# Kernel tuning notes

Hardware: AMD Instinct MI355X
Metric: run time of the kernel (lower is better)

The kernel has to match this reference:

```python
import jax, jax.numpy as jnp
import numpy as np

N_HEADS = 16
EMBED_DIM = 1024

def setup_inputs() -> dict:
    key = jax.random.key(0)
    ks = jax.random.split(key, 5)
    C = EMBED_DIM
    s = 0.02
    return {
        "x": jax.random.normal(ks[0], (4, 2048, C), dtype=jnp.float32),
        "W_attn": jax.random.normal(ks[1], (C, 3 * C), dtype=jnp.float32) * s,
        "b_attn": jnp.zeros((3 * C,), dtype=jnp.float32),
        "W_proj": jax.random.normal(ks[2], (C, C), dtype=jnp.float32) * s,
        "b_proj": jnp.zeros((C,), dtype=jnp.float32),
    }

def reference(x, W_attn, b_attn, W_proj, b_proj):
    B, T, C = x.shape
    H = N_HEADS
    hd = C // H
    qkv = x @ W_attn + b_attn                      # [B,T,3C]
    q, k, v = jnp.split(qkv, 3, axis=-1)
    # [B,T,C] -> [B,H,T,hd]
    q = q.reshape(B, T, H, hd).transpose(0, 2, 1, 3)
    k = k.reshape(B, T, H, hd).transpose(0, 2, 1, 3)
    v = v.reshape(B, T, H, hd).transpose(0, 2, 1, 3)
    scale = 1.0 / np.sqrt(hd).astype(np.float32)
    att = jnp.einsum("bhqd,bhkd->bhqk", q, k) * scale   # [B,H,T,T]
    causal = jnp.tril(jnp.ones((T, T), dtype=bool))
    att = jnp.where(causal[None, None], att, -jnp.inf)
    att = jax.nn.softmax(att, axis=-1)
    y = jnp.einsum("bhqk,bhkd->bhqd", att, v)            # [B,H,T,hd]
    y = y.transpose(0, 2, 1, 3).reshape(B, T, C)
    return y @ W_proj + b_proj
```

## Files before the change

### kernel.cpp

```cpp
#include <hip/hip_runtime.h>
#include <stdint.h>

#define T_ 2048
#define C_ 1024
#define H_ 16
#define HD_ 64

typedef __attribute__((ext_vector_type(8))) short bf16x8;
typedef __attribute__((ext_vector_type(4))) float f32x4;

#define EXP2F(x) __builtin_amdgcn_exp2f(x)

__device__ __forceinline__ unsigned short f2b(float f) {
  union { float f; unsigned u; } v; v.f = f;
  return (unsigned short)((v.u + 0x7fffu + ((v.u >> 16) & 1u)) >> 16);
}

__global__ void cvt_f32_bf16(const float* __restrict__ in, unsigned short* __restrict__ out, int n4) {
  int stride = gridDim.x * blockDim.x;
  for (int i = blockIdx.x * blockDim.x + threadIdx.x; i < n4; i += stride) {
    float4 v = ((const float4*)in)[i];
    ushort4 o;
    o.x = f2b(v.x); o.y = f2b(v.y); o.z = f2b(v.z); o.w = f2b(v.w);
    ((ushort4*)out)[i] = o;
  }
}

__global__ void transpose_cvt(const float* __restrict__ in, unsigned short* __restrict__ out, int K, int N) {
  __shared__ float tile[32][33];
  int k0 = blockIdx.x * 32, n0 = blockIdx.y * 32;
  int tx = threadIdx.x & 31, ty = threadIdx.x >> 5;
#pragma unroll
  for (int i = 0; i < 4; ++i)
    tile[ty + i*8][tx] = in[(size_t)(k0 + ty + i*8) * N + n0 + tx];
  __syncthreads();
#pragma unroll
  for (int i = 0; i < 4; ++i)
    out[(size_t)(n0 + ty + i*8) * K + k0 + tx] = f2b(tile[tx][ty + i*8]);
}

#define GL16(g, l) __builtin_amdgcn_global_load_lds((const __attribute__((address_space(1))) void*)(g), (__attribute__((address_space(3))) void*)(l), 16, 0, 0)

template<int EPI>
__global__ __launch_bounds__(256) void gemm128(
    const unsigned short* __restrict__ A,
    const unsigned short* __restrict__ Bt,
    const float* __restrict__ bias,
    float* __restrict__ outF,
    unsigned short* __restrict__ outQ,
    unsigned short* __restrict__ outK,
    unsigned short* __restrict__ outV,
    int M, int N, int K)
{
  __shared__ __align__(16) unsigned short Al[2][128*32];
  __shared__ __align__(16) unsigned short Bl[2][128*32];
  const int tid = threadIdx.x, lane = tid & 63, w = tid >> 6;
  const int wm = w >> 1, wn = w & 1;
  const int m0 = blockIdx.x * 128, n0 = blockIdx.y * 128;

  f32x4 acc[4][4];
#pragma unroll
  for (int i = 0; i < 4; ++i)
#pragma unroll
    for (int j = 0; j < 4; ++j)
      acc[i][j] = (f32x4)0.0f;

  const int NT = K >> 5;
  const int srow = lane >> 2;
  const int punit = lane & 3;

#pragma unroll
  for (int i = 0; i < 2; ++i) {
    int chunk = w*2 + i;
    int row = chunk*16 + srow;
    int lu = punit ^ ((row >> 1) & 3);
    GL16(A  + (size_t)(m0 + row) * K + lu*8, &Al[0][chunk*512]);
    GL16(Bt + (size_t)(n0 + row) * K + lu*8, &Bl[0][chunk*512]);
  }
  __syncthreads();

  for (int kt = 0; kt < NT; ++kt) {
    if (kt + 1 < NT) {
      int nb = (kt+1) & 1;
#pragma unroll
      for (int i = 0; i < 2; ++i) {
        int chunk = w*2 + i;
        int row = chunk*16 + srow;
        int lu = punit ^ ((row >> 1) & 3);
        GL16(A  + (size_t)(m0 + row) * K + ((kt+1) << 5) + lu*8, &Al[nb][chunk*512]);
        GL16(Bt + (size_t)(n0 + row) * K + ((kt+1) << 5) + lu*8, &Bl[nb][chunk*512]);
      }
    }
    {
      const int cb = kt & 1;
      const int r16 = lane & 15, u = lane >> 4;
      bf16x8 af[4], bfr[4];
#pragma unroll
      for (int f = 0; f < 4; ++f) {
        int ra = wm*64 + f*16 + r16;
        af[f]  = *(const bf16x8*)&Al[cb][ra*32 + ((u ^ ((ra>>1)&3)) << 3)];
        int rb = wn*64 + f*16 + r16;
        bfr[f] = *(const bf16x8*)&Bl[cb][rb*32 + ((u ^ ((rb>>1)&3)) << 3)];
      }
#pragma unroll
      for (int i = 0; i < 4; ++i)
#pragma unroll
        for (int j = 0; j < 4; ++j)
          acc[i][j] = __builtin_amdgcn_mfma_f32_16x16x32_bf16(af[i], bfr[j], acc[i][j], 0, 0, 0);
    }
    __syncthreads();
  }

  const int u = lane >> 4, r16 = lane & 15;
#pragma unroll
  for (int i = 0; i < 4; ++i) {
    int rbase = m0 + wm*64 + i*16 + u*4;
#pragma unroll
    for (int j = 0; j < 4; ++j) {
      int col = n0 + wn*64 + j*16 + r16;
      float bv = bias[col];
      if (EPI == 0) {
#pragma unroll
        for (int r = 0; r < 4; ++r)
          outF[(size_t)(rbase + r) * N + col] = acc[i][j][r] + bv;
      } else {
        int sec = col >> 10, c = col & 1023, h = c >> 6, d = c & 63;
        int b = rbase >> 11, t = rbase & (T_ - 1);
        if (sec == 0) {
#pragma unroll
          for (int r = 0; r < 4; ++r)
            outQ[(((size_t)b*H_ + h)*T_ + (t + r))*HD_ + d] = f2b((acc[i][j][r] + bv) * 0.18033688f);
        } else if (sec == 1) {
#pragma unroll
          for (int r = 0; r < 4; ++r)
            outK[(((size_t)b*H_ + h)*T_ + (t + r))*HD_ + d] = f2b(acc[i][j][r] + bv);
        } else {
          ushort4 pk;
          pk.x = f2b(acc[i][j][0] + bv);
          pk.y = f2b(acc[i][j][1] + bv);
          pk.z = f2b(acc[i][j][2] + bv);
          pk.w = f2b(acc[i][j][3] + bv);
          *(ushort4*)&outV[(((size_t)b*H_ + h)*HD_ + d)*T_ + t] = pk;
        }
      }
    }
  }
}

__global__ __launch_bounds__(256) void attn_fused(
    const unsigned short* __restrict__ Q,
    const unsigned short* __restrict__ Kc,
    const unsigned short* __restrict__ Vt,
    unsigned short* __restrict__ Y)
{
  __shared__ __align__(16) unsigned short Pl[4][32*64];
  const int tid = threadIdx.x, lane = tid & 63, w = tid >> 6;
  const int r16 = lane & 15, u = lane >> 4;

  const int l = blockIdx.x;
  const int xcd = l & 7, slot = l >> 3;
  const int xr = slot & 15, grp = slot >> 4;
  const int qtile = (xr & 1) ? (xr >> 1) : (15 - (xr >> 1));
  const int bh = xcd + grp * 8;
  const int q0 = qtile * 128;
  const int b = bh >> 4, h = bh & 15;
  const int qw = q0 + w * 32;

  const unsigned short* Qb = Q  + ((size_t)bh*T_ + qw)*HD_;
  const unsigned short* Kb = Kc + (size_t)bh*T_*HD_;
  const unsigned short* Vb = Vt + (size_t)bh*HD_*T_;

  bf16x8 qf[2][2];
#pragma unroll
  for (int fm = 0; fm < 2; ++fm)
#pragma unroll
    for (int kk = 0; kk < 2; ++kk)
      qf[fm][kk] = *(const bf16x8*)&Qb[(size_t)(fm*16 + r16)*HD_ + kk*32 + u*8];

  f32x4 o[2][4];
  float mr[2][4], lr[2][4];
#pragma unroll
  for (int fm = 0; fm < 2; ++fm) {
#pragma unroll
    for (int fd = 0; fd < 4; ++fd) o[fm][fd] = (f32x4)0.0f;
#pragma unroll
    for (int jr = 0; jr < 4; ++jr) { mr[fm][jr] = -1e30f; lr[fm][jr] = 0.0f; }
  }

  const int ntiles = (qw >> 6) + 1;

  for (int t = 0; t < ntiles; ++t) {
    const int kv0 = t * 64;
    f32x4 s[2][4];
#pragma unroll
    for (int fm = 0; fm < 2; ++fm)
#pragma unroll
      for (int fn = 0; fn < 4; ++fn) s[fm][fn] = (f32x4)0.0f;
#pragma unroll
    for (int fn = 0; fn < 4; ++fn) {
      const size_t krow = (size_t)(kv0 + fn*16 + r16) * HD_;
#pragma unroll
      for (int kk = 0; kk < 2; ++kk) {
        bf16x8 kf = *(const bf16x8*)&Kb[krow + kk*32 + u*8];
        s[0][fn] = __builtin_amdgcn_mfma_f32_16x16x32_bf16(qf[0][kk], kf, s[0][fn], 0,0,0);
        s[1][fn] = __builtin_amdgcn_mfma_f32_16x16x32_bf16(qf[1][kk], kf, s[1][fn], 0,0,0);
      }
    }
    if (kv0 + 63 > qw) {
#pragma unroll
      for (int fm = 0; fm < 2; ++fm)
#pragma unroll
        for (int fn = 0; fn < 4; ++fn) {
          int kv = kv0 + fn*16 + r16;
#pragma unroll
          for (int jr = 0; jr < 4; ++jr) {
            int q = qw + fm*16 + u*4 + jr;
            if (kv > q) s[fm][fn][jr] = -1e30f;
          }
        }
    }
    float mt[2][4];
#pragma unroll
    for (int fm = 0; fm < 2; ++fm)
#pragma unroll
      for (int jr = 0; jr < 4; ++jr)
        mt[fm][jr] = fmaxf(fmaxf(s[fm][0][jr], s[fm][1][jr]), fmaxf(s[fm][2][jr], s[fm][3][jr]));
#pragma unroll
    for (int msk = 1; msk < 16; msk <<= 1)
#pragma unroll
      for (int fm = 0; fm < 2; ++fm)
#pragma unroll
        for (int jr = 0; jr < 4; ++jr)
          mt[fm][jr] = fmaxf(mt[fm][jr], __shfl_xor(mt[fm][jr], msk, 64));
    float alpha[2][4], rs[2][4];
#pragma unroll
    for (int fm = 0; fm < 2; ++fm)
#pragma unroll
      for (int jr = 0; jr < 4; ++jr) {
        float mn = fmaxf(mr[fm][jr], mt[fm][jr]);
        alpha[fm][jr] = EXP2F(mr[fm][jr] - mn);
        mr[fm][jr] = mn;
        rs[fm][jr] = 0.0f;
      }
#pragma unroll
    for (int fm = 0; fm < 2; ++fm)
#pragma unroll
      for (int fn = 0; fn < 4; ++fn) {
        int kvc = fn*16 + r16;
#pragma unroll
        for (int jr = 0; jr < 4; ++jr) {
          float p = EXP2F(s[fm][fn][jr] - mr[fm][jr]);
          rs[fm][jr] += p;
          int qloc = fm*16 + u*4 + jr;
          int boff = qloc*128 + ((kvc*2) ^ ((qloc & 7) << 4));
          *(unsigned short*)((char*)&Pl[w][0] + boff) = f2b(p);
        }
      }
#pragma unroll
    for (int msk = 1; msk < 16; msk <<= 1)
#pragma unroll
      for (int fm = 0; fm < 2; ++fm)
#pragma unroll
        for (int jr = 0; jr < 4; ++jr)
          rs[fm][jr] += __shfl_xor(rs[fm][jr], msk, 64);
#pragma unroll
    for (int fm = 0; fm < 2; ++fm)
#pragma unroll
      for (int jr = 0; jr < 4; ++jr)
        lr[fm][jr] = lr[fm][jr]*alpha[fm][jr] + rs[fm][jr];
#pragma unroll
    for (int fm = 0; fm < 2; ++fm)
#pragma unroll
      for (int fd = 0; fd < 4; ++fd)
#pragma unroll
        for (int jr = 0; jr < 4; ++jr)
          o[fm][fd][jr] *= alpha[fm][jr];
#pragma unroll
    for (int kks = 0; kks < 2; ++kks) {
      bf16x8 pa[2];
#pragma unroll
      for (int fm = 0; fm < 2; ++fm) {
        int rq = fm*16 + r16;
        int un = (kks*4 + u) ^ (rq & 7);
        pa[fm] = *(const bf16x8*)&Pl[w][rq*64 + un*8];
      }
#pragma unroll
      for (int fd = 0; fd < 4; ++fd) {
        bf16x8 vf = *(const bf16x8*)&Vb[(size_t)(fd*16 + r16)*T_ + kv0 + kks*32 + u*8];
        o[0][fd] = __builtin_amdgcn_mfma_f32_16x16x32_bf16(pa[0], vf, o[0][fd], 0,0,0);
        o[1][fd] = __builtin_amdgcn_mfma_f32_16x16x32_bf16(pa[1], vf, o[1][fd], 0,0,0);
      }
    }
  }

#pragma unroll
  for (int fm = 0; fm < 2; ++fm) {
    int tb = qw + fm*16 + u*4;
#pragma unroll
    for (int jr = 0; jr < 4; ++jr) {
      float inv = 1.0f / lr[fm][jr];
      int tt = tb + jr;
#pragma unroll
      for (int fd = 0; fd < 4; ++fd) {
        int c = h*64 + fd*16 + r16;
        Y[((size_t)b*T_ + tt)*C_ + c] = f2b(o[fm][fd][jr] * inv);
      }
    }
  }
}

extern "C" void kernel_launch(void* const* d_in, const int* in_sizes, int n_in,
                              void* d_out, int out_size, void* d_ws, size_t ws_size,
                              hipStream_t stream) {
  const float* x      = (const float*)d_in[0];
  const float* W_attn = (const float*)d_in[1];
  const float* b_attn = (const float*)d_in[2];
  const float* W_proj = (const float*)d_in[3];
  const float* b_proj = (const float*)d_in[4];
  float* out = (float*)d_out;

  char* ws = (char*)d_ws;
  unsigned short* xb  = (unsigned short*)(ws);
  unsigned short* Wta = (unsigned short*)(ws + (16u << 20));
  unsigned short* Wtp = (unsigned short*)(ws + (22u << 20));
  unsigned short* qb  = (unsigned short*)(ws + (24u << 20));
  unsigned short* kb  = (unsigned short*)(ws + (40u << 20));
  unsigned short* vtb = (unsigned short*)(ws + (56u << 20));

  cvt_f32_bf16<<<2048, 256, 0, stream>>>(x, xb, (4 * T_ * C_) / 4);
  transpose_cvt<<<dim3(C_/32, (3*C_)/32), 256, 0, stream>>>(W_attn, Wta, C_, 3*C_);
  transpose_cvt<<<dim3(C_/32, C_/32), 256, 0, stream>>>(W_proj, Wtp, C_, C_);
  gemm128<1><<<dim3(64, 24), 256, 0, stream>>>(xb, Wta, b_attn, nullptr, qb, kb, vtb, 8192, 3072, 1024);
  attn_fused<<<1024, 256, 0, stream>>>(qb, kb, vtb, xb);
  gemm128<0><<<dim3(64, 8), 256, 0, stream>>>(xb, Wtp, b_proj, out, nullptr, nullptr, nullptr, 8192, 1024, 1024);
}
```

Before: 411.0 us.

## Shrink attention tile to 16 query rows per wave and double the grid

Each wave now handles 16 query rows instead of 32, so a block covers 64 queries and the grid grows to 2048 blocks with remapped causal tile ordering. Register and LDS use per block drop, and launch bounds ask for 5 waves per SIMD to raise occupancy. The first V fragment is prefetched before the softmax to hide load latency. In exchange, K/V tiles are reused across half as many queries, which raises global/L2 traffic per unit of compute.

New measurement: 679.1 us. +65.2%, slower.

```diff
diff --git a/kernel.cpp b/kernel.cpp
--- a/kernel.cpp
+++ b/kernel.cpp
@@ -147,164 +147,137 @@
   }
 }
 
-__global__ __launch_bounds__(256) void attn_fused(
+__global__ __launch_bounds__(256, 5) void attn_fused(
     const unsigned short* __restrict__ Q,
     const unsigned short* __restrict__ Kc,
     const unsigned short* __restrict__ Vt,
     unsigned short* __restrict__ Y)
 {
-  __shared__ __align__(16) unsigned short Pl[4][32*64];
+  __shared__ __align__(16) unsigned short Pl[4][16*64];
   const int tid = threadIdx.x, lane = tid & 63, w = tid >> 6;
   const int r16 = lane & 15, u = lane >> 4;
 
   const int l = blockIdx.x;
   const int xcd = l & 7, slot = l >> 3;
-  const int xr = slot & 15, grp = slot >> 4;
-  const int qtile = (xr & 1) ? (xr >> 1) : (15 - (xr >> 1));
+  const int xr = slot & 31, grp = slot >> 5;
+  const int qtile = (xr & 1) ? (xr >> 1) : (31 - (xr >> 1));
   const int bh = xcd + grp * 8;
-  const int q0 = qtile * 128;
+  const int q0 = qtile * 64;
   const int b = bh >> 4, h = bh & 15;
-  const int qw = q0 + w * 32;
+  const int qw = q0 + w * 16;
 
   const unsigned short* Qb = Q  + ((size_t)bh*T_ + qw)*HD_;
   const unsigned short* Kb = Kc + (size_t)bh*T_*HD_;
   const unsigned short* Vb = Vt + (size_t)bh*HD_*T_;
 
-  bf16x8 qf[2][2];
-#pragma unroll
-  for (int fm = 0; fm < 2; ++fm)
-#pragma unroll
-    for (int kk = 0; kk < 2; ++kk)
-      qf[fm][kk] = *(const bf16x8*)&Qb[(size_t)(fm*16 + r16)*HD_ + kk*32 + u*8];
-
-  f32x4 o[2][4];
-  float mr[2][4], lr[2][4];
-#pragma unroll
-  for (int fm = 0; fm < 2; ++fm) {
-#pragma unroll
-    for (int fd = 0; fd < 4; ++fd) o[fm][fd] = (f32x4)0.0f;
-#pragma unroll
-    for (int jr = 0; jr < 4; ++jr) { mr[fm][jr] = -1e30f; lr[fm][jr] = 0.0f; }
-  }
+  bf16x8 qf[2];
+#pragma unroll
+  for (int kk = 0; kk < 2; ++kk)
+    qf[kk] = *(const bf16x8*)&Qb[(size_t)r16*HD_ + kk*32 + u*8];
+
+  f32x4 o[4];
+  float mr[4], lr[4];
+#pragma unroll
+  for (int fd = 0; fd < 4; ++fd) o[fd] = (f32x4)0.0f;
+#pragma unroll
+  for (int jr = 0; jr < 4; ++jr) { mr[jr] = -1e30f; lr[jr] = 0.0f; }
 
   const int ntiles = (qw >> 6) + 1;
 
   for (int t = 0; t < ntiles; ++t) {
     const int kv0 = t * 64;
-    f32x4 s[2][4];
-#pragma unroll
-    for (int fm = 0; fm < 2; ++fm)
-#pragma unroll
-      for (int fn = 0; fn < 4; ++fn) s[fm][fn] = (f32x4)0.0f;
+    f32x4 s[4];
+#pragma unroll
+    for (int fn = 0; fn < 4; ++fn) s[fn] = (f32x4)0.0f;
 #pragma unroll
     for (int fn = 0; fn < 4; ++fn) {
       const size_t krow = (size_t)(kv0 + fn*16 + r16) * HD_;
 #pragma unroll
       for (int kk = 0; kk < 2; ++kk) {
         bf16x8 kf = *(const bf16x8*)&Kb[krow + kk*32 + u*8];
-        s[0][fn] = __builtin_amdgcn_mfma_f32_16x16x32_bf16(qf[0][kk], kf, s[0][fn], 0,0,0);
-        s[1][fn] = __builtin_amdgcn_mfma_f32_16x16x32_bf16(qf[1][kk], kf, s[1][fn], 0,0,0);
-      }
-    }
+        s[fn] = __builtin_amdgcn_mfma_f32_16x16x32_bf16(qf[kk], kf, s[fn], 0,0,0);
+      }
+    }
+    bf16x8 vf0[4];
+#pragma unroll
+    for (int fd = 0; fd < 4; ++fd)
+      vf0[fd] = *(const bf16x8*)&Vb[(size_t)(fd*16 + r16)*T_ + kv0 + u*8];
+
     if (kv0 + 63 > qw) {
 #pragma unroll
-      for (int fm = 0; fm < 2; ++fm)
-#pragma unroll
-        for (int fn = 0; fn < 4; ++fn) {
-          int kv = kv0 + fn*16 + r16;
-#pragma unroll
-          for (int jr = 0; jr < 4; ++jr) {
-            int q = qw + fm*16 + u*4 + jr;
-            if (kv > q) s[fm][fn][jr] = -1e30f;
-          }
+      for (int fn = 0; fn < 4; ++fn) {
+        int kv = kv0 + fn*16 + r16;
+#pragma unroll
+        for (int jr = 0; jr < 4; ++jr) {
+          int q = qw + u*4 + jr;
+          if (kv > q) s[fn][jr] = -1e30f;
         }
-    }
-    float mt[2][4];
-#pragma unroll
-    for (int fm = 0; fm < 2; ++fm)
+      }
+    }
+    float mt[4];
+#pragma unroll
+    for (int jr = 0; jr < 4; ++jr)
+      mt[jr] = fmaxf(fmaxf(s[0][jr], s[1][jr]), fmaxf(s[2][jr], s[3][jr]));
+#pragma unroll
+    for (int msk = 1; msk < 16; msk <<= 1)
 #pragma unroll
       for (int jr = 0; jr < 4; ++jr)
-        mt[fm][jr] = fmaxf(fmaxf(s[fm][0][jr], s[fm][1][jr]), fmaxf(s[fm][2][jr], s[fm][3][jr]));
+        mt[jr] = fmaxf(mt[jr], __shfl_xor(mt[jr], msk, 64));
+    float alpha[4], rs[4];
+#pragma unroll
+    for (int jr = 0; jr < 4; ++jr) {
+      float mn = fmaxf(mr[jr], mt[jr]);
+      alpha[jr] = EXP2F(mr[jr] - mn);
+      mr[jr] = mn;
+      rs[jr] = 0.0f;
+    }
+#pragma unroll
+    for (int fn = 0; fn < 4; ++fn) {
+      int kvc = fn*16 + r16;
+#pragma unroll
+      for (int jr = 0; jr < 4; ++jr) {
+        float p = EXP2F(s[fn][jr] - mr[jr]);
+        rs[jr] += p;
+        int qloc = u*4 + jr;
+        int boff = qloc*128 + ((kvc*2) ^ ((qloc & 7) << 4));
+        *(unsigned short*)((char*)&Pl[w][0] + boff) = f2b(p);
+      }
+    }
 #pragma unroll
     for (int msk = 1; msk < 16; msk <<= 1)
 #pragma unroll
-      for (int fm = 0; fm < 2; ++fm)
-#pragma unroll
-        for (int jr = 0; jr < 4; ++jr)
-          mt[fm][jr] = fmaxf(mt[fm][jr], __shfl_xor(mt[fm][jr], msk, 64));
-    float alpha[2][4], rs[2][4];
-#pragma unroll
-    for (int fm = 0; fm < 2; ++fm)
-#pragma unroll
-      for (int jr = 0; jr < 4; ++jr) {
-        float mn = fmaxf(mr[fm][jr], mt[fm][jr]);
-        alpha[fm][jr] = EXP2F(mr[fm][jr] - mn);
-        mr[fm][jr] = mn;
-        rs[fm][jr] = 0.0f;
-      }
-#pragma unroll
-    for (int fm = 0; fm < 2; ++fm)
-#pragma unroll
-      for (int fn = 0; fn < 4; ++fn) {
-        int kvc = fn*16 + r16;
-#pragma unroll
-        for (int jr = 0; jr < 4; ++jr) {
-          float p = EXP2F(s[fm][fn][jr] - mr[fm][jr]);
-          rs[fm][jr] += p;
-          int qloc = fm*16 + u*4 + jr;
-          int boff = qloc*128 + ((kvc*2) ^ ((qloc & 7) << 4));
-          *(unsigned short*)((char*)&Pl[w][0] + boff) = f2b(p);
-        }
-      }
-#pragma unroll
-    for (int msk = 1; msk < 16; msk <<= 1)
-#pragma unroll
-      for (int fm = 0; fm < 2; ++fm)
-#pragma unroll
-        for (int jr = 0; jr < 4; ++jr)
-          rs[fm][jr] += __shfl_xor(rs[fm][jr], msk, 64);
-#pragma unroll
-    for (int fm = 0; fm < 2; ++fm)
-#pragma unroll
       for (int jr = 0; jr < 4; ++jr)
-        lr[fm][jr] = lr[fm][jr]*alpha[fm][jr] + rs[fm][jr];
-#pragma unroll
-    for (int fm = 0; fm < 2; ++fm)
-#pragma unroll
-      for (int fd = 0; fd < 4; ++fd)
-#pragma unroll
-        for (int jr = 0; jr < 4; ++jr)
-          o[fm][fd][jr] *= alpha[fm][jr];
+        rs[jr] += __shfl_xor(rs[jr], msk, 64);
+#pragma unroll
+    for (int jr = 0; jr < 4; ++jr)
+      lr[jr] = lr[jr]*alpha[jr] + rs[jr];
+#pragma unroll
+    for (int fd = 0; fd < 4; ++fd)
+#pragma unroll
+      for (int jr = 0; jr < 4; ++jr)
+        o[fd][jr] *= alpha[jr];
 #pragma unroll
     for (int kks = 0; kks < 2; ++kks) {
-      bf16x8 pa[2];
-#pragma unroll
-      for (int fm = 0; fm < 2; ++fm) {
-        int rq = fm*16 + r16;
-        int un = (kks*4 + u) ^ (rq & 7);
-        pa[fm] = *(const bf16x8*)&Pl[w][rq*64 + un*8];
-      }
+      int un = (kks*4 + u) ^ (r16 & 7);
+      bf16x8 pa = *(const bf16x8*)&Pl[w][r16*64 + un*8];
 #pragma unroll
       for (int fd = 0; fd < 4; ++fd) {
-        bf16x8 vf = *(const bf16x8*)&Vb[(size_t)(fd*16 + r16)*T_ + kv0 + kks*32 + u*8];
-        o[0][fd] = __builtin_amdgcn_mfma_f32_16x16x32_bf16(pa[0], vf, o[0][fd], 0,0,0);
-        o[1][fd] = __builtin_amdgcn_mfma_f32_16x16x32_bf16(pa[1], vf, o[1][fd], 0,0,0);
-      }
-    }
-  }
-
-#pragma unroll
-  for (int fm = 0; fm < 2; ++fm) {
-    int tb = qw + fm*16 + u*4;
-#pragma unroll
-    for (int jr = 0; jr < 4; ++jr) {
-      float inv = 1.0f / lr[fm][jr];
-      int tt = tb + jr;
-#pragma unroll
-      for (int fd = 0; fd < 4; ++fd) {
-        int c = h*64 + fd*16 + r16;
-        Y[((size_t)b*T_ + tt)*C_ + c] = f2b(o[fm][fd][jr] * inv);
-      }
+        bf16x8 vf = kks ? *(const bf16x8*)&Vb[(size_t)(fd*16 + r16)*T_ + kv0 + 32 + u*8]
+                        : vf0[fd];
+        o[fd] = __builtin_amdgcn_mfma_f32_16x16x32_bf16(pa, vf, o[fd], 0,0,0);
+      }
+    }
+  }
+
+  int tb = qw + u*4;
+#pragma unroll
+  for (int jr = 0; jr < 4; ++jr) {
+    float inv = 1.0f / lr[jr];
+    int tt = tb + jr;
+#pragma unroll
+    for (int fd = 0; fd < 4; ++fd) {
+      int c = h*64 + fd*16 + r16;
+      Y[((size_t)b*T_ + tt)*C_ + c] = f2b(o[fd][jr] * inv);
     }
   }
 }
@@ -331,6 +304,6 @@
   transpose_cvt<<<dim3(C_/32, (3*C_)/32), 256, 0, stream>>>(W_attn, Wta, C_, 3*C_);
   transpose_cvt<<<dim3(C_/32, C_/32), 256, 0, stream>>>(W_proj, Wtp, C_, C_);
   gemm128<1><<<dim3(64, 24), 256, 0, stream>>>(xb, Wta, b_attn, nullptr, qb, kb, vtb, 8192, 3072, 1024);
-  attn_fused<<<1024, 256, 0, stream>>>(qb, kb, vtb, xb);
+  attn_fused<<<2048, 256, 0, stream>>>(qb, kb, vtb, xb);
   gemm128<0><<<dim3(64, 8), 256, 0, stream>>>(xb, Wtp, b_proj, out, nullptr, nullptr, nullptr, 8192, 1024, 1024);
 }
```
